# Performance work log

Measured on AMD Instinct MI355X. Metric: run time of the kernel, lower is better.

## Reference

```python
import jax, jax.numpy as jnp
import numpy as np


def setup_inputs() -> dict:
    key = jax.random.key(0)
    bs, n_heads, ch, length = 4, 8, 64, 2048
    width = 3 * n_heads * ch  # 1536
    qkv = jax.random.normal(key, (bs, width, length), dtype=jnp.float32)
    return {"qkv": qkv, "n_heads": n_heads}


def reference(qkv, n_heads):
    bs, width, length = qkv.shape
    ch = width // (3 * n_heads)
    # reshape to (bs*heads, 3*ch, length) then split into q, k, v of (B, ch, L)
    qkv_r = qkv.reshape(bs * n_heads, 3 * ch, length)
    q, k, v = qkv_r[:, :ch], qkv_r[:, ch:2 * ch], qkv_r[:, 2 * ch:]
    scale = ch ** (-0.5)
    # weight = bmm(q^T, k) * scale -> (B, L_q, L_k)
    weight = jnp.einsum('bct,bcs->bts', q, k) * scale
    weight = jax.nn.softmax(weight.astype(jnp.float32), axis=-1).astype(qkv.dtype)
    # a = bmm(v, weight^T) -> (B, ch, L)
    a = jnp.einsum('bcs,bts->bct', v, weight)
    return a.reshape(bs, n_heads * ch, length)
```

## Files before the change

kernel.cpp:

```cpp
#include <hip/hip_runtime.h>

typedef __bf16 bf16;
typedef __attribute__((ext_vector_type(8)))  __bf16 bf16x8;
typedef __attribute__((ext_vector_type(16))) float  f32x16;

#define LEN   2048
#define CH    64
#define HEADS 32

union PackU { unsigned u[4]; bf16x8 v; };

static __device__ inline unsigned pack2(float lo, float hi) {
  union { bf16 h[2]; unsigned u; } p;
  p.h[0] = (bf16)lo; p.h[1] = (bf16)hi;
  return p.u;
}

static __device__ inline void async_cp16(const bf16* g, bf16* l) {
  __builtin_amdgcn_global_load_lds(
      (const __attribute__((address_space(1))) void*)g,
      (__attribute__((address_space(3))) void*)l, 16, 0, 0);
}

__global__ __launch_bounds__(256) void prep_kernel(const float* __restrict__ qkv,
                                                   bf16* __restrict__ ws) {
  __shared__ float tile[64][65];
  const int tIdx = blockIdx.x;
  const int g    = blockIdx.y;
  const int tid  = threadIdx.x;
  const int s0   = tIdx * 64;
  const float* K = qkv + (g * 192 + 64)  * LEN;
  const float* V = qkv + (g * 192 + 128) * LEN;

  {
    const int c0 = tid >> 6, s = tid & 63;
#pragma unroll
    for (int i = 0; i < 16; ++i) {
      const int c = c0 + i * 4;
      tile[c][s] = K[c * LEN + s0 + s];
    }
  }
  __syncthreads();

  bf16* dst = ws + ((size_t)g * 32 + tIdx) * 8192;
#pragma unroll
  for (int it = 0; it < 2; ++it) {
    const int c2  = tid + it * 256;
    const int row = c2 >> 3, cx = c2 & 7;
    const int cb  = (cx ^ (row & 7)) * 8;
    bf16x8 o;
#pragma unroll
    for (int j = 0; j < 8; ++j) o[j] = (bf16)tile[cb + j][row];
    *(bf16x8*)(dst + c2 * 8) = o;
  }
#pragma unroll
  for (int it = 0; it < 2; ++it) {
    const int c2  = tid + it * 256;
    const int row = c2 >> 3, cx = c2 & 7;
    const int k8  = cx ^ (row & 7);
    const int pa  = 32 * (k8 >> 2) + 8 * ((k8 >> 1) & 1) + 4 * (k8 & 1);
    const float* src = V + row * LEN + s0 + pa;
    const float4 a = *(const float4*)src;
    const float4 b = *(const float4*)(src + 16);
    bf16x8 o;
    o[0] = (bf16)a.x; o[1] = (bf16)a.y; o[2] = (bf16)a.z; o[3] = (bf16)a.w;
    o[4] = (bf16)b.x; o[5] = (bf16)b.y; o[6] = (bf16)b.z; o[7] = (bf16)b.w;
    *(bf16x8*)(dst + 4096 + c2 * 8) = o;
  }
}

__global__ __launch_bounds__(512, 2) void attn_kernel(const float* __restrict__ qkv,
                                                      const bf16* __restrict__ ws,
                                                      float* __restrict__ out) {
  __shared__ __align__(16) bf16 stg[32768];

  const int tid  = threadIdx.x;
  const int lane = tid & 63;
  const int w    = tid >> 6;
  const int wg   = w & 3;
  const int sg   = w >> 2;
  const int n    = lane & 31;
  const int h    = lane >> 5;
  const int g    = blockIdx.x & 31;
  const int jb   = blockIdx.x >> 5;
  const int t0   = jb * 256 + wg * 64;

  const bf16* wsg = ws + (size_t)g * (32 * 8192);

  auto stage = [&](int i) {
    const bf16* src = wsg + i * 8192;
    bf16* dst = stg + (i & 3) * 8192;
#pragma unroll
    for (int it = 0; it < 2; ++it) {
      const int chunk = w * 128 + it * 64 + lane;
      async_cp16(src + chunk * 8, dst + chunk * 8);
    }
  };
  stage(0); stage(1);

  const float qs = 0.125f * 1.44269504088896340736f;
  const float* Q = qkv + g * (192 * LEN);
  bf16x8 qf[2][4];
#pragma unroll
  for (int e = 0; e < 2; ++e)
#pragma unroll
    for (int kb = 0; kb < 4; ++kb)
#pragma unroll
      for (int jj = 0; jj < 8; ++jj)
        qf[e][kb][jj] = (bf16)(Q[(kb * 16 + h * 8 + jj) * LEN + t0 + e * 32 + n] * qs);

  f32x16 o_acc[2][2];
#pragma unroll
  for (int e = 0; e < 2; ++e)
#pragma unroll
    for (int mb = 0; mb < 2; ++mb)
#pragma unroll
      for (int r = 0; r < 16; ++r) o_acc[e][mb][r] = 0.f;
  float l_acc[2] = {0.f, 0.f};

  for (int p = 0; p < 16; ++p) {
    __syncthreads();
    if (p < 15) { stage(2 * p + 2); stage(2 * p + 3); }
    const bf16* ktl = stg + ((2 * p + sg) & 3) * 8192;
    const bf16* vl  = ktl + 4096;

    f32x16 sf[2][2];
#pragma unroll
    for (int e = 0; e < 2; ++e)
#pragma unroll
      for (int mb = 0; mb < 2; ++mb)
#pragma unroll
        for (int r = 0; r < 16; ++r) sf[e][mb][r] = 0.f;
#pragma unroll
    for (int kb = 0; kb < 4; ++kb)
#pragma unroll
      for (int mb = 0; mb < 2; ++mb) {
        const bf16x8 a = *(const bf16x8*)(ktl + (mb * 32 + n) * 64 + (((kb * 2 + h) ^ (n & 7)) * 8));
        sf[0][mb] = __builtin_amdgcn_mfma_f32_32x32x16_bf16(a, qf[0][kb], sf[0][mb], 0, 0, 0);
        sf[1][mb] = __builtin_amdgcn_mfma_f32_32x32x16_bf16(a, qf[1][kb], sf[1][mb], 0, 0, 0);
      }

    PackU frag[2][4];
#pragma unroll
    for (int e = 0; e < 2; ++e) {
      float ls = 0.f;
#pragma unroll
      for (int mb = 0; mb < 2; ++mb)
#pragma unroll
        for (int u = 0; u < 4; ++u) {
          const float p0 = __builtin_amdgcn_exp2f(sf[e][mb][4 * u + 0]);
          const float p1 = __builtin_amdgcn_exp2f(sf[e][mb][4 * u + 1]);
          const float p2 = __builtin_amdgcn_exp2f(sf[e][mb][4 * u + 2]);
          const float p3 = __builtin_amdgcn_exp2f(sf[e][mb][4 * u + 3]);
          ls += (p0 + p1) + (p2 + p3);
          const int kb   = 2 * mb + (u & 1);
          const int base = 2 * (u >> 1);
          frag[e][kb].u[base]     = pack2(p0, p1);
          frag[e][kb].u[base + 1] = pack2(p2, p3);
        }
      l_acc[e] += ls;
    }

#pragma unroll
    for (int kbs = 0; kbs < 4; ++kbs)
#pragma unroll
      for (int mbo = 0; mbo < 2; ++mbo) {
        const bf16x8 a = *(const bf16x8*)(vl + (mbo * 32 + n) * 64 + (((kbs * 2 + h) ^ (n & 7)) * 8));
        o_acc[0][mbo] = __builtin_amdgcn_mfma_f32_32x32x16_bf16(a, frag[0][kbs].v, o_acc[0][mbo], 0, 0, 0);
        o_acc[1][mbo] = __builtin_amdgcn_mfma_f32_32x32x16_bf16(a, frag[1][kbs].v, o_acc[1][mbo], 0, 0, 0);
      }
  }

  float lt[2];
#pragma unroll
  for (int e = 0; e < 2; ++e) lt[e] = l_acc[e] + __shfl_xor(l_acc[e], 32);

  float* fx = (float*)stg;
  float* lx = fx + 15104;

#pragma unroll
  for (int mbo = 0; mbo < 2; ++mbo) {
    __syncthreads();
    if (sg == 1) {
#pragma unroll
      for (int e = 0; e < 2; ++e)
#pragma unroll
        for (int u = 0; u < 4; ++u) {
          float4 st;
          st.x = o_acc[e][mbo][4 * u + 0];
          st.y = o_acc[e][mbo][4 * u + 1];
          st.z = o_acc[e][mbo][4 * u + 2];
          st.w = o_acc[e][mbo][4 * u + 3];
          *(float4*)&fx[wg * 2304 + (e * 32 + n) * 36 + 8 * u + 4 * h] = st;
        }
      if (mbo == 0 && h == 0) {
        lx[wg * 64 + n]      = lt[0];
        lx[wg * 64 + 32 + n] = lt[1];
      }
    }
    __syncthreads();
    if (sg == 0) {
#pragma unroll
      for (int e = 0; e < 2; ++e)
#pragma unroll
        for (int u = 0; u < 4; ++u) {
          const float4 q = *(const float4*)&fx[wg * 2304 + (e * 32 + n) * 36 + 8 * u + 4 * h];
          o_acc[e][mbo][4 * u + 0] += q.x;
          o_acc[e][mbo][4 * u + 1] += q.y;
          o_acc[e][mbo][4 * u + 2] += q.z;
          o_acc[e][mbo][4 * u + 3] += q.w;
        }
    }
  }

  if (sg == 0) {
    float inv[2];
#pragma unroll
    for (int e = 0; e < 2; ++e) inv[e] = 1.0f / (lt[e] + lx[wg * 64 + e * 32 + n]);
    float* og = out + g * (CH * LEN);
#pragma unroll
    for (int e = 0; e < 2; ++e)
#pragma unroll
      for (int mbo = 0; mbo < 2; ++mbo)
#pragma unroll
        for (int r = 0; r < 16; ++r) {
          const int c = 32 * mbo + (r & 3) + 8 * (r >> 2) + 4 * h;
          og[c * LEN + t0 + e * 32 + n] = o_acc[e][mbo][r] * inv[e];
        }
  }
}

extern "C" void kernel_launch(void* const* d_in, const int* in_sizes, int n_in,
                              void* d_out, int out_size, void* d_ws, size_t ws_size,
                              hipStream_t stream) {
  const float* qkv = (const float*)d_in[0];
  float* out = (float*)d_out;
  bf16* ws = (bf16*)d_ws;

  prep_kernel<<<dim3(32, HEADS), 256, 0, stream>>>(qkv, ws);
  attn_kernel<<<dim3(256), 512, 0, stream>>>(qkv, ws, out);
}
```

Measured before the change: 128.0 us.

## Shrink attention blocks, stage only K in LDS, read V directly from global

Blocks drop from 512 to 256 threads with 128 query columns each, so the grid doubles to 512 blocks. Only K tiles are double-buffered in LDS, and each split-K group now streams its own half of the key range. V fragments are loaded straight from global memory (unswizzled layout from prep) into registers. The epilogue merges the two split-K partial sums in one LDS exchange instead of two. The aim is to raise occupancy and cut LDS traffic, at the cost of exposed global-memory latency on the V loads and higher register pressure.

```diff
diff --git a/kernel.cpp b/kernel.cpp
--- a/kernel.cpp
+++ b/kernel.cpp
@@ -56,8 +56,7 @@
 #pragma unroll
   for (int it = 0; it < 2; ++it) {
     const int c2  = tid + it * 256;
-    const int row = c2 >> 3, cx = c2 & 7;
-    const int k8  = cx ^ (row & 7);
+    const int row = c2 >> 3, k8 = c2 & 7;
     const int pa  = 32 * (k8 >> 2) + 8 * ((k8 >> 1) & 1) + 4 * (k8 & 1);
     const float* src = V + row * LEN + s0 + pa;
     const float4 a = *(const float4*)src;
@@ -69,34 +68,36 @@
   }
 }
 
-__global__ __launch_bounds__(512, 2) void attn_kernel(const float* __restrict__ qkv,
+__global__ __launch_bounds__(256, 2) void attn_kernel(const float* __restrict__ qkv,
                                                       const bf16* __restrict__ ws,
                                                       float* __restrict__ out) {
-  __shared__ __align__(16) bf16 stg[32768];
+  __shared__ __align__(16) unsigned char lds_raw[35392];
+  bf16* stg = (bf16*)lds_raw;
 
   const int tid  = threadIdx.x;
   const int lane = tid & 63;
   const int w    = tid >> 6;
-  const int wg   = w & 3;
-  const int sg   = w >> 2;
+  const int wg   = w & 1;
+  const int sg   = w >> 1;
   const int n    = lane & 31;
   const int h    = lane >> 5;
   const int g    = blockIdx.x & 31;
   const int jb   = blockIdx.x >> 5;
-  const int t0   = jb * 256 + wg * 64;
-
-  const bf16* wsg = ws + (size_t)g * (32 * 8192);
+  const int t0   = jb * 128 + wg * 64;
+
+  const bf16* wsg    = ws + (size_t)g * (32 * 8192);
+  const bf16* tiles0 = wsg + (size_t)(sg * 16) * 8192;
 
   auto stage = [&](int i) {
-    const bf16* src = wsg + i * 8192;
-    bf16* dst = stg + (i & 3) * 8192;
-#pragma unroll
-    for (int it = 0; it < 2; ++it) {
-      const int chunk = w * 128 + it * 64 + lane;
-      async_cp16(src + chunk * 8, dst + chunk * 8);
+    const bf16* src = tiles0 + i * 8192;
+    bf16* dstp = stg + (sg * 2 + (i & 1)) * 4096;
+#pragma unroll
+    for (int it = 0; it < 4; ++it) {
+      const int chunk = wg * 256 + it * 64 + lane;
+      async_cp16(src + chunk * 8, dstp + chunk * 8);
     }
   };
-  stage(0); stage(1);
+  stage(0);
 
   const float qs = 0.125f * 1.44269504088896340736f;
   const float* Q = qkv + g * (192 * LEN);
@@ -118,11 +119,19 @@
       for (int r = 0; r < 16; ++r) o_acc[e][mb][r] = 0.f;
   float l_acc[2] = {0.f, 0.f};
 
-  for (int p = 0; p < 16; ++p) {
+  for (int i = 0; i < 16; ++i) {
     __syncthreads();
-    if (p < 15) { stage(2 * p + 2); stage(2 * p + 3); }
-    const bf16* ktl = stg + ((2 * p + sg) & 3) * 8192;
-    const bf16* vl  = ktl + 4096;
+    if (i < 15) stage(i + 1);
+
+    const bf16* vt = tiles0 + i * 8192 + 4096;
+    bf16x8 vf[4][2];
+#pragma unroll
+    for (int kbs = 0; kbs < 4; ++kbs)
+#pragma unroll
+      for (int mbo = 0; mbo < 2; ++mbo)
+        vf[kbs][mbo] = *(const bf16x8*)(vt + (mbo * 32 + n) * 64 + (kbs * 2 + h) * 8);
+
+    const bf16* ktl = stg + (sg * 2 + (i & 1)) * 4096;
 
     f32x16 sf[2][2];
 #pragma unroll
@@ -165,9 +174,8 @@
     for (int kbs = 0; kbs < 4; ++kbs)
 #pragma unroll
       for (int mbo = 0; mbo < 2; ++mbo) {
-        const bf16x8 a = *(const bf16x8*)(vl + (mbo * 32 + n) * 64 + (((kbs * 2 + h) ^ (n & 7)) * 8));
-        o_acc[0][mbo] = __builtin_amdgcn_mfma_f32_32x32x16_bf16(a, frag[0][kbs].v, o_acc[0][mbo], 0, 0, 0);
-        o_acc[1][mbo] = __builtin_amdgcn_mfma_f32_32x32x16_bf16(a, frag[1][kbs].v, o_acc[1][mbo], 0, 0, 0);
+        o_acc[0][mbo] = __builtin_amdgcn_mfma_f32_32x32x16_bf16(vf[kbs][mbo], frag[0][kbs].v, o_acc[0][mbo], 0, 0, 0);
+        o_acc[1][mbo] = __builtin_amdgcn_mfma_f32_32x32x16_bf16(vf[kbs][mbo], frag[1][kbs].v, o_acc[1][mbo], 0, 0, 0);
       }
   }
 
@@ -175,15 +183,15 @@
 #pragma unroll
   for (int e = 0; e < 2; ++e) lt[e] = l_acc[e] + __shfl_xor(l_acc[e], 32);
 
-  float* fx = (float*)stg;
-  float* lx = fx + 15104;
-
-#pragma unroll
-  for (int mbo = 0; mbo < 2; ++mbo) {
-    __syncthreads();
-    if (sg == 1) {
-#pragma unroll
-      for (int e = 0; e < 2; ++e)
+  float* ebuf = (float*)lds_raw;
+  float* lbuf = (float*)(lds_raw + 34816);
+
+  __syncthreads();
+  if (sg == 1) {
+#pragma unroll
+    for (int e = 0; e < 2; ++e)
+#pragma unroll
+      for (int mbo = 0; mbo < 2; ++mbo)
 #pragma unroll
         for (int u = 0; u < 4; ++u) {
           float4 st;
@@ -191,41 +199,35 @@
           st.y = o_acc[e][mbo][4 * u + 1];
           st.z = o_acc[e][mbo][4 * u + 2];
           st.w = o_acc[e][mbo][4 * u + 3];
-          *(float4*)&fx[wg * 2304 + (e * 32 + n) * 36 + 8 * u + 4 * h] = st;
+          *(float4*)&ebuf[wg * 4352 + (e * 32 + n) * 68 + mbo * 32 + 8 * u + 4 * h] = st;
         }
-      if (mbo == 0 && h == 0) {
-        lx[wg * 64 + n]      = lt[0];
-        lx[wg * 64 + 32 + n] = lt[1];
-      }
-    }
-    __syncthreads();
-    if (sg == 0) {
-#pragma unroll
-      for (int e = 0; e < 2; ++e)
-#pragma unroll
-        for (int u = 0; u < 4; ++u) {
-          const float4 q = *(const float4*)&fx[wg * 2304 + (e * 32 + n) * 36 + 8 * u + 4 * h];
-          o_acc[e][mbo][4 * u + 0] += q.x;
-          o_acc[e][mbo][4 * u + 1] += q.y;
-          o_acc[e][mbo][4 * u + 2] += q.z;
-          o_acc[e][mbo][4 * u + 3] += q.w;
-        }
-    }
-  }
-
+    if (h == 0) {
+      lbuf[wg * 64 + n]      = lt[0];
+      lbuf[wg * 64 + 32 + n] = lt[1];
+    }
+  }
+  __syncthreads();
   if (sg == 0) {
     float inv[2];
 #pragma unroll
-    for (int e = 0; e < 2; ++e) inv[e] = 1.0f / (lt[e] + lx[wg * 64 + e * 32 + n]);
+    for (int e = 0; e < 2; ++e) inv[e] = 1.0f / (lt[e] + lbuf[wg * 64 + e * 32 + n]);
     float* og = out + g * (CH * LEN);
 #pragma unroll
     for (int e = 0; e < 2; ++e)
 #pragma unroll
       for (int mbo = 0; mbo < 2; ++mbo)
 #pragma unroll
-        for (int r = 0; r < 16; ++r) {
-          const int c = 32 * mbo + (r & 3) + 8 * (r >> 2) + 4 * h;
-          og[c * LEN + t0 + e * 32 + n] = o_acc[e][mbo][r] * inv[e];
+        for (int u = 0; u < 4; ++u) {
+          const float4 q = *(const float4*)&ebuf[wg * 4352 + (e * 32 + n) * 68 + mbo * 32 + 8 * u + 4 * h];
+          const float r0 = (o_acc[e][mbo][4 * u + 0] + q.x) * inv[e];
+          const float r1 = (o_acc[e][mbo][4 * u + 1] + q.y) * inv[e];
+          const float r2 = (o_acc[e][mbo][4 * u + 2] + q.z) * inv[e];
+          const float r3 = (o_acc[e][mbo][4 * u + 3] + q.w) * inv[e];
+          const int cb = mbo * 32 + 8 * u + 4 * h;
+          og[(cb + 0) * LEN + t0 + e * 32 + n] = r0;
+          og[(cb + 1) * LEN + t0 + e * 32 + n] = r1;
+          og[(cb + 2) * LEN + t0 + e * 32 + n] = r2;
+          og[(cb + 3) * LEN + t0 + e * 32 + n] = r3;
         }
   }
 }
@@ -238,5 +240,5 @@
   bf16* ws = (bf16*)d_ws;
 
   prep_kernel<<<dim3(32, HEADS), 256, 0, stream>>>(qkv, ws);
-  attn_kernel<<<dim3(256), 512, 0, stream>>>(qkv, ws, out);
-}
+  attn_kernel<<<dim3(512), 256, 0, stream>>>(qkv, ws, out);
+}
```

Measured after the change: 128.7 us. About the same (+0.5%).
